# Optimization experiments

Hardware: AMD Instinct MI355X
Metric: run time of the kernel (lower is better)

The kernel has to match this reference:

```python
import jax, jax.numpy as jnp
import numpy as np

N_NODES = 100000
N_EDGES = 1600000
D = 128
L = 3


def setup_inputs() -> dict:
    key = jax.random.key(0)
    k1, k2, k3 = jax.random.split(key, 3)
    edge_index = jax.random.randint(k1, (2, N_EDGES), 0, N_NODES, dtype=jnp.int64)
    emb = jax.random.normal(k2, (N_NODES, D), dtype=jnp.float32)
    # Glorot-style scale for the per-layer linear weights
    Ws = jax.random.normal(k3, (L, D, D), dtype=jnp.float32) * (1.0 / np.sqrt(D))
    bs = jnp.zeros((L, D), dtype=jnp.float32)
    return {"edge_index": edge_index, "emb": emb, "Ws": Ws, "bs": bs}


def _gcn_forward(emb, Ws, bs, edge_index):
    n = emb.shape[0]
    self_loop = jnp.arange(n, dtype=edge_index.dtype)
    # PyG GCNConv adds self-loops and uses symmetric normalization
    row = jnp.concatenate([edge_index[0], self_loop])  # source nodes
    col = jnp.concatenate([edge_index[1], self_loop])  # target nodes
    deg = jax.ops.segment_sum(jnp.ones(row.shape[0], dtype=emb.dtype), col, num_segments=n)
    deg_inv_sqrt = jnp.where(deg > 0, jax.lax.rsqrt(jnp.maximum(deg, 1.0)), 0.0)
    norm = deg_inv_sqrt[row] * deg_inv_sqrt[col]  # [E+N]

    x = emb
    for l in range(Ws.shape[0]):
        h = x @ Ws[l]                              # [N, D] linear transform
        msg = h[row] * norm[:, None]               # gather + scale [E+N, D]
        x = jax.ops.segment_sum(msg, col, num_segments=n) + bs[l]  # scatter-add
        x = jax.nn.relu(x)                         # dropout is identity in eval
    return x


def reference(edge_index, emb, Ws, bs) -> jnp.ndarray:
    return _gcn_forward(emb, Ws, bs, edge_index)
```

## Files before the change

kernel.cpp:

```cpp
#include <hip/hip_runtime.h>
#include <hip/hip_fp16.h>
#include <cstdint>
#include <cstddef>

#define N_NODES 100000
#define N_EDGES 1600000
#define D 128
#define NLAYERS 3
#define NB 3125
#define NBLK_E 128
#define EPB 12500
#define ENT_CAP 1024


__global__ __launch_bounds__(512) void hist1_kernel(const int* __restrict__ col,
                                                    int* __restrict__ hmat) {
    __shared__ int hist[NB];
    int b = blockIdx.x, t = threadIdx.x;
    for (int j = t; j < NB; j += 512) hist[j] = 0;
    __syncthreads();
    int base = b * EPB;
    for (int i = t; i < EPB; i += 512) {
        int c = col[base + i];
        atomicAdd(&hist[c >> 5], 1);
    }
    __syncthreads();
    for (int j = t; j < NB; j += 512) hmat[b * NB + j] = hist[j];
}

__global__ void btot_kernel(const int* __restrict__ hmat, int* __restrict__ btot) {
    int j = blockIdx.x * 256 + threadIdx.x;
    if (j < NB) {
        int s = 0;
        for (int b = 0; b < NBLK_E; b++) s += hmat[b * NB + j];
        btot[j] = s;
    }
}

__global__ void bscan_kernel(const int* __restrict__ btot, int* __restrict__ bstart, int nb, int e) {
    __shared__ int lsum[1024];
    int t = threadIdx.x;
    int vals[4];
    int v0 = 0;
#pragma unroll
    for (int j = 0; j < 4; j++) {
        int idx = t * 4 + j;
        int c = (idx < nb) ? btot[idx] : 0;
        vals[j] = c;
        v0 += c;
    }
    lsum[t] = v0;
    __syncthreads();
    for (int off = 1; off < 1024; off <<= 1) {
        int x = (t >= off) ? lsum[t - off] : 0;
        __syncthreads();
        lsum[t] += x;
        __syncthreads();
    }
    int base = lsum[t] - v0;
#pragma unroll
    for (int j = 0; j < 4; j++) {
        int idx = t * 4 + j;
        if (idx < nb) {
            bstart[idx] = base;
            base += vals[j];
        }
    }
    if (t == 0) bstart[nb] = e;
}

__global__ void hoff_kernel(const int* __restrict__ hmat, const int* __restrict__ bstart,
                            int* __restrict__ hoff) {
    int j = blockIdx.x * 256 + threadIdx.x;
    if (j < NB) {
        int run = bstart[j];
        for (int b = 0; b < NBLK_E; b++) {
            hoff[b * NB + j] = run;
            run += hmat[b * NB + j];
        }
    }
}

__global__ __launch_bounds__(512) void scatter_kernel(const int* __restrict__ row,
                                                      const int* __restrict__ col,
                                                      const int* __restrict__ hoff,
                                                      unsigned* __restrict__ bucketbuf) {
    __shared__ int cur[NB];
    int b = blockIdx.x, t = threadIdx.x;
    for (int j = t; j < NB; j += 512) cur[j] = hoff[b * NB + j];
    __syncthreads();
    int base = b * EPB;
    for (int i = t; i < EPB; i += 512) {
        int r = row[base + i], c = col[base + i];
        int pos = atomicAdd(&cur[c >> 5], 1);
        bucketbuf[pos] = ((unsigned)r << 5) | (unsigned)(c & 31);
    }
}

__global__ void fill2_kernel(const unsigned* __restrict__ bucketbuf, const int* __restrict__ bstart,
                             int* __restrict__ offsets, float* __restrict__ dinv,
                             int* __restrict__ src, int n, int e) {
    __shared__ unsigned ent[ENT_CAP];
    __shared__ int hist[32];
    __shared__ int cur[32];
    __shared__ int loff[32];
    int b = blockIdx.x, t = threadIdx.x;
    int s0 = bstart[b];
    int cnt = bstart[b + 1] - s0;
    if (cnt > ENT_CAP) cnt = ENT_CAP;
    if (t < 32) hist[t] = 0;
    __syncthreads();
    for (int i = t; i < cnt; i += 256) {
        unsigned v = bucketbuf[s0 + i];
        ent[i] = v;
        atomicAdd(&hist[v & 31], 1);
    }
    __syncthreads();
    if (t == 0) {
        int run = s0;
#pragma unroll
        for (int j = 0; j < 32; j++) {
            loff[j] = run;
            run += hist[j];
        }
    }
    __syncthreads();
    if (t < 32) {
        int node = b * 32 + t;
        int o = loff[t];
        offsets[node] = o;
        cur[t] = o;
        dinv[node] = rsqrtf((float)(hist[t] + 1));
    }
    if (b == 0 && t == 0) offsets[n] = e;
    __syncthreads();
    for (int i = t; i < cnt; i += 256) {
        unsigned v = ent[i];
        int pos = atomicAdd(&cur[v & 31], 1);
        src[pos] = (int)(v >> 5);
    }
}


__global__ void cast_kernel(const float2* __restrict__ in, __half2* __restrict__ out, int n2) {
    int i = blockIdx.x * 256 + threadIdx.x;
    if (i < n2) {
        float2 v = in[i];
        out[i] = __floats2half2_rn(v.x, v.y);
    }
}

__global__ void agg_kernel(const __half2* __restrict__ xh, const int* __restrict__ offs,
                           const int* __restrict__ src, const float* __restrict__ dinv,
                           float* __restrict__ out) {
    int v = blockIdx.x;
    int f = threadIdx.x;
    float dv = dinv[v];
    float2 xv = __half22float2(xh[(size_t)v * 64 + f]);
    float ax = dv * xv.x;
    float ay = dv * xv.y;
    int i = offs[v], s1 = offs[v + 1];
    for (; i + 3 < s1; i += 4) {
        int sA = src[i], sB = src[i + 1], sC = src[i + 2], sD = src[i + 3];
        float wA = dinv[sA], wB = dinv[sB], wC = dinv[sC], wD = dinv[sD];
        float2 xA = __half22float2(xh[(size_t)sA * 64 + f]);
        float2 xB = __half22float2(xh[(size_t)sB * 64 + f]);
        float2 xC = __half22float2(xh[(size_t)sC * 64 + f]);
        float2 xD = __half22float2(xh[(size_t)sD * 64 + f]);
        ax += xA.x * wA + xB.x * wB + xC.x * wC + xD.x * wD;
        ay += xA.y * wA + xB.y * wB + xC.y * wC + xD.y * wD;
    }
    for (; i < s1; i++) {
        int sA = src[i];
        float wA = dinv[sA];
        float2 xA = __half22float2(xh[(size_t)sA * 64 + f]);
        ax += xA.x * wA;
        ay += xA.y * wA;
    }
    float2 r;
    r.x = dv * ax;
    r.y = dv * ay;
    ((float2*)out)[(size_t)v * 64 + f] = r;
}

__global__ __launch_bounds__(256, 2) void gemm_bias_relu_kernel(
    const float* __restrict__ A, const float* __restrict__ W,
    const float* __restrict__ bias, float* __restrict__ out,
    __half2* __restrict__ xh_out, int write_h) {
    __shared__ float sW[128 * 128];
    __shared__ float sX[32 * 128];
    int t = threadIdx.x;
    int tx = t & 31;
    int ty = t >> 5;
    int row0 = blockIdx.x * 32;

    const float4* W4 = (const float4*)W;
    float4* sW4 = (float4*)sW;
#pragma unroll
    for (int i = 0; i < 16; i++) sW4[t + 256 * i] = W4[t + 256 * i];

    const float4* A4 = (const float4*)A;
    float4* sX4 = (float4*)sX;
#pragma unroll
    for (int i = 0; i < 4; i++) {
        int c = t + 256 * i;
        int r = c >> 5, kc = c & 31;
        sX4[r * 32 + kc] = A4[(size_t)(row0 + r) * 32 + kc];
    }
    __syncthreads();

    float4 acc[4];
#pragma unroll
    for (int r = 0; r < 4; r++) acc[r] = make_float4(0.f, 0.f, 0.f, 0.f);

#define FMA4(a, s, b) a.x += (s) * (b).x; a.y += (s) * (b).y; a.z += (s) * (b).z; a.w += (s) * (b).w;
#pragma unroll 4
    for (int k0 = 0; k0 < 128; k0 += 4) {
        float4 b0 = *(const float4*)&sW[(k0 + 0) * 128 + tx * 4];
        float4 b1 = *(const float4*)&sW[(k0 + 1) * 128 + tx * 4];
        float4 b2 = *(const float4*)&sW[(k0 + 2) * 128 + tx * 4];
        float4 b3 = *(const float4*)&sW[(k0 + 3) * 128 + tx * 4];
#pragma unroll
        for (int r = 0; r < 4; r++) {
            float4 a = *(const float4*)&sX[(ty * 4 + r) * 128 + k0];
            FMA4(acc[r], a.x, b0)
            FMA4(acc[r], a.y, b1)
            FMA4(acc[r], a.z, b2)
            FMA4(acc[r], a.w, b3)
        }
    }
#undef FMA4

    float4 bb = ((const float4*)bias)[tx];
#pragma unroll
    for (int r = 0; r < 4; r++) {
        float4 o;
        o.x = fmaxf(acc[r].x + bb.x, 0.0f);
        o.y = fmaxf(acc[r].y + bb.y, 0.0f);
        o.z = fmaxf(acc[r].z + bb.z, 0.0f);
        o.w = fmaxf(acc[r].w + bb.w, 0.0f);
        size_t rowi = (size_t)(row0 + ty * 4 + r);
        ((float4*)out)[rowi * 32 + tx] = o;
        if (write_h) {
            xh_out[rowi * 64 + tx * 2] = __floats2half2_rn(o.x, o.y);
            xh_out[rowi * 64 + tx * 2 + 1] = __floats2half2_rn(o.z, o.w);
        }
    }
}


extern "C" void kernel_launch(void* const* d_in, const int* in_sizes, int n_in,
                              void* d_out, int out_size, void* d_ws, size_t ws_size,
                              hipStream_t stream) {
    const int* edge = (const int*)d_in[0];
    const float* emb = (const float*)d_in[1];
    const float* Ws = (const float*)d_in[2];
    const float* bs = (const float*)d_in[3];
    float* out = (float*)d_out;

    const int n = N_NODES, e = N_EDGES;
    const int* row = edge;
    const int* col = edge + e;

    char* p = (char*)d_ws;
    float* aggbuf = (float*)p;
    int* hmat = (int*)p;
    int* hoff = hmat + (size_t)NBLK_E * NB;
    p += (size_t)n * D * 4;
    __half2* xh = (__half2*)p;
    unsigned* bucketbuf = (unsigned*)p;
    p += (size_t)n * D * 2;
    int* csr_src  = (int*)p;    p += (size_t)e * 4;
    float* dinv   = (float*)p;  p += (size_t)n * 4;
    int* offsets  = (int*)p;    p += (size_t)(n + 1) * 4;
    int* btot     = (int*)p;    p += (size_t)NB * 4;
    int* bstart   = (int*)p;    p += (size_t)(NB + 1) * 4;

    hist1_kernel<<<NBLK_E, 512, 0, stream>>>(col, hmat);
    btot_kernel<<<(NB + 255) / 256, 256, 0, stream>>>(hmat, btot);
    bscan_kernel<<<1, 1024, 0, stream>>>(btot, bstart, NB, e);
    hoff_kernel<<<(NB + 255) / 256, 256, 0, stream>>>(hmat, bstart, hoff);
    scatter_kernel<<<NBLK_E, 512, 0, stream>>>(row, col, hoff, bucketbuf);
    fill2_kernel<<<NB, 256, 0, stream>>>(bucketbuf, bstart, offsets, dinv, csr_src, n, e);

    int n2 = n * 64;
    cast_kernel<<<(n2 + 255) / 256, 256, 0, stream>>>((const float2*)emb, xh, n2);

    for (int l = 0; l < NLAYERS; l++) {
        agg_kernel<<<n, 64, 0, stream>>>(xh, offsets, csr_src, dinv, aggbuf);
        gemm_bias_relu_kernel<<<n / 32, 256, 0, stream>>>(
            aggbuf, Ws + (size_t)l * D * D, bs + (size_t)l * D, out,
            xh, (l < NLAYERS - 1) ? 1 : 0);
    }
}
```

Measured before the change: 541.1 us.

## Prescale features by source dinv and widen aggregation gathers to 16-byte loads

Source-side normalization is folded into the stored half-precision features: the cast and the GEMM epilogue multiply by dinv before writing. This removes the per-edge dinv gather in aggregation. The aggregation kernel is restructured to one wave per node, with four edge groups of 16 lanes each loading 8 halves (16 bytes) per neighbor, followed by a cross-group shuffle reduction. The histogram kernel is also vectorized with int4 loads. The trade-off is that fp16 now stores prescaled values, which slightly changes rounding.

```diff
diff --git a/kernel.cpp b/kernel.cpp
--- a/kernel.cpp
+++ b/kernel.cpp
@@ -12,6 +12,8 @@
 #define EPB 12500
 #define ENT_CAP 1024
 
+typedef __attribute__((ext_vector_type(8))) _Float16 half8;
+
 
 __global__ __launch_bounds__(512) void hist1_kernel(const int* __restrict__ col,
                                                     int* __restrict__ hmat) {
@@ -19,10 +21,13 @@
     int b = blockIdx.x, t = threadIdx.x;
     for (int j = t; j < NB; j += 512) hist[j] = 0;
     __syncthreads();
-    int base = b * EPB;
-    for (int i = t; i < EPB; i += 512) {
-        int c = col[base + i];
-        atomicAdd(&hist[c >> 5], 1);
+    const int4* col4 = (const int4*)(col + b * EPB);
+    for (int i = t; i < EPB / 4; i += 512) {
+        int4 c = col4[i];
+        atomicAdd(&hist[c.x >> 5], 1);
+        atomicAdd(&hist[c.y >> 5], 1);
+        atomicAdd(&hist[c.z >> 5], 1);
+        atomicAdd(&hist[c.w >> 5], 1);
     }
     __syncthreads();
     for (int j = t; j < NB; j += 512) hmat[b * NB + j] = hist[j];
@@ -142,51 +147,71 @@
 }
 
 
-__global__ void cast_kernel(const float2* __restrict__ in, __half2* __restrict__ out, int n2) {
+__global__ void cast_kernel(const float2* __restrict__ in, const float* __restrict__ dinv,
+                            __half2* __restrict__ out, int n2) {
     int i = blockIdx.x * 256 + threadIdx.x;
     if (i < n2) {
+        float dv = dinv[i >> 6];
         float2 v = in[i];
-        out[i] = __floats2half2_rn(v.x, v.y);
-    }
-}
-
-__global__ void agg_kernel(const __half2* __restrict__ xh, const int* __restrict__ offs,
-                           const int* __restrict__ src, const float* __restrict__ dinv,
-                           float* __restrict__ out) {
-    int v = blockIdx.x;
-    int f = threadIdx.x;
-    float dv = dinv[v];
-    float2 xv = __half22float2(xh[(size_t)v * 64 + f]);
-    float ax = dv * xv.x;
-    float ay = dv * xv.y;
-    int i = offs[v], s1 = offs[v + 1];
-    for (; i + 3 < s1; i += 4) {
-        int sA = src[i], sB = src[i + 1], sC = src[i + 2], sD = src[i + 3];
-        float wA = dinv[sA], wB = dinv[sB], wC = dinv[sC], wD = dinv[sD];
-        float2 xA = __half22float2(xh[(size_t)sA * 64 + f]);
-        float2 xB = __half22float2(xh[(size_t)sB * 64 + f]);
-        float2 xC = __half22float2(xh[(size_t)sC * 64 + f]);
-        float2 xD = __half22float2(xh[(size_t)sD * 64 + f]);
-        ax += xA.x * wA + xB.x * wB + xC.x * wC + xD.x * wD;
-        ay += xA.y * wA + xB.y * wB + xC.y * wC + xD.y * wD;
-    }
-    for (; i < s1; i++) {
+        out[i] = __floats2half2_rn(dv * v.x, dv * v.y);
+    }
+}
+
+__global__ __launch_bounds__(256) void agg_kernel(const __half* __restrict__ xs,
+                                                  const int* __restrict__ offs,
+                                                  const int* __restrict__ src,
+                                                  const float* __restrict__ dinv,
+                                                  float* __restrict__ out) {
+    int wave = threadIdx.x >> 6;
+    int lane = threadIdx.x & 63;
+    int v = blockIdx.x * 4 + wave;
+    int g = lane >> 4, f = lane & 15;
+    const char* xb = (const char*)xs;
+
+    float acc[8] = {0.f, 0.f, 0.f, 0.f, 0.f, 0.f, 0.f, 0.f};
+    if (g == 0) {
+        half8 hv = *(const half8*)(xb + ((size_t)v << 8) + (f << 4));
+#pragma unroll
+        for (int j = 0; j < 8; j++) acc[j] += (float)hv[j];
+    }
+
+    int o0 = offs[v], o1 = offs[v + 1];
+    int i = o0 + g;
+    for (; i + 4 < o1; i += 8) {
+        int sA = src[i], sB = src[i + 4];
+        half8 hA = *(const half8*)(xb + ((size_t)sA << 8) + (f << 4));
+        half8 hB = *(const half8*)(xb + ((size_t)sB << 8) + (f << 4));
+#pragma unroll
+        for (int j = 0; j < 8; j++) acc[j] += (float)hA[j] + (float)hB[j];
+    }
+    if (i < o1) {
         int sA = src[i];
-        float wA = dinv[sA];
-        float2 xA = __half22float2(xh[(size_t)sA * 64 + f]);
-        ax += xA.x * wA;
-        ay += xA.y * wA;
-    }
-    float2 r;
-    r.x = dv * ax;
-    r.y = dv * ay;
-    ((float2*)out)[(size_t)v * 64 + f] = r;
+        half8 hA = *(const half8*)(xb + ((size_t)sA << 8) + (f << 4));
+#pragma unroll
+        for (int j = 0; j < 8; j++) acc[j] += (float)hA[j];
+    }
+
+#pragma unroll
+    for (int j = 0; j < 8; j++) {
+        acc[j] += __shfl_xor(acc[j], 16, 64);
+        acc[j] += __shfl_xor(acc[j], 32, 64);
+    }
+
+    if (g < 2) {
+        float dv = dinv[v];
+        float4 w4;
+        w4.x = dv * acc[g * 4 + 0];
+        w4.y = dv * acc[g * 4 + 1];
+        w4.z = dv * acc[g * 4 + 2];
+        w4.w = dv * acc[g * 4 + 3];
+        *(float4*)(out + (size_t)v * 128 + f * 8 + g * 4) = w4;
+    }
 }
 
 __global__ __launch_bounds__(256, 2) void gemm_bias_relu_kernel(
     const float* __restrict__ A, const float* __restrict__ W,
-    const float* __restrict__ bias, float* __restrict__ out,
-    __half2* __restrict__ xh_out, int write_h) {
+    const float* __restrict__ bias, const float* __restrict__ dinv,
+    float* __restrict__ out, __half2* __restrict__ xh_out, int write_h) {
     __shared__ float sW[128 * 128];
     __shared__ float sX[32 * 128];
     int t = threadIdx.x;
@@ -242,8 +267,9 @@
         size_t rowi = (size_t)(row0 + ty * 4 + r);
         ((float4*)out)[rowi * 32 + tx] = o;
         if (write_h) {
-            xh_out[rowi * 64 + tx * 2] = __floats2half2_rn(o.x, o.y);
-            xh_out[rowi * 64 + tx * 2 + 1] = __floats2half2_rn(o.z, o.w);
+            float dv = dinv[rowi];
+            xh_out[rowi * 64 + tx * 2] = __floats2half2_rn(dv * o.x, dv * o.y);
+            xh_out[rowi * 64 + tx * 2 + 1] = __floats2half2_rn(dv * o.z, dv * o.w);
         }
     }
 }
@@ -284,12 +310,12 @@
     fill2_kernel<<<NB, 256, 0, stream>>>(bucketbuf, bstart, offsets, dinv, csr_src, n, e);
 
     int n2 = n * 64;
-    cast_kernel<<<(n2 + 255) / 256, 256, 0, stream>>>((const float2*)emb, xh, n2);
+    cast_kernel<<<(n2 + 255) / 256, 256, 0, stream>>>((const float2*)emb, dinv, xh, n2);
 
     for (int l = 0; l < NLAYERS; l++) {
-        agg_kernel<<<n, 64, 0, stream>>>(xh, offsets, csr_src, dinv, aggbuf);
+        agg_kernel<<<n / 4, 256, 0, stream>>>((const __half*)xh, offsets, csr_src, dinv, aggbuf);
         gemm_bias_relu_kernel<<<n / 32, 256, 0, stream>>>(
-            aggbuf, Ws + (size_t)l * D * D, bs + (size_t)l * D, out,
+            aggbuf, Ws + (size_t)l * D * D, bs + (size_t)l * D, dinv, out,
             xh, (l < NLAYERS - 1) ? 1 : 0);
     }
 }
```

Result: no change. 544.1 us (+0.6%).
